# Optimization experiments

Hardware: AMD Instinct MI355X
Metric: run time of the kernel (lower is better)

## Reference

```python
import jax, jax.numpy as jnp
import numpy as np

B, T, C, H = 8, 2048, 256, 4
D = C // H  # head_dim = 64
SCALE = D ** -0.5


def setup_inputs() -> dict:
    key = jax.random.key(0)
    ks = jax.random.split(key, 5)
    return {
        "x": jax.random.normal(ks[0], (B, T, C), dtype=jnp.float32),
        "Wqkv": jax.random.normal(ks[1], (C, 3 * C), dtype=jnp.float32) * (C ** -0.5),
        "bqkv": jax.random.normal(ks[2], (3 * C,), dtype=jnp.float32) * 0.02,
        "Wproj": jax.random.normal(ks[3], (C, C), dtype=jnp.float32) * (C ** -0.5),
        "bproj": jax.random.normal(ks[4], (C,), dtype=jnp.float32) * 0.02,
    }


def reference(x, Wqkv, bqkv, Wproj, bproj):
    b, t, c = x.shape
    # QKV projection -> (3, B, H, T, D) matching torch permute(2,0,3,1,4)
    qkv = (x @ Wqkv + bqkv).reshape(b, t, 3, H, D)
    qkv = jnp.transpose(qkv, (2, 0, 3, 1, 4))
    q, k, v = qkv[0], qkv[1], qkv[2]  # each (B, H, T, D)
    # Full T x T scores (faithful to the original non-fused implementation)
    attn = jnp.einsum("bhqd,bhkd->bhqk", q, k) * SCALE
    causal = jnp.triu(jnp.ones((t, t), dtype=bool), k=1)  # True above diagonal
    attn = jnp.where(causal, -jnp.inf, attn)
    attn = jax.nn.softmax(attn, axis=-1)
    # dropout is identity in eval mode
    out = jnp.einsum("bhqk,bhkd->bhqd", attn, v)  # (B, H, T, D)
    out = jnp.transpose(out, (0, 2, 1, 3)).reshape(b, t, c)
    return out @ Wproj + bproj
```

## Files before the change

### kernel.cpp

```cpp
#include <hip/hip_runtime.h>
#include <hip/hip_bf16.h>
#include <math.h>

#define BATCH 8
#define SEQ   2048
#define CH    256
#define NH    4
#define HD    64
#define NQB   (SEQ / 64)
#define QSCALE 0.18033688011112042f

typedef short  bfrag  __attribute__((ext_vector_type(8)));
typedef float  ffrag  __attribute__((ext_vector_type(4)));
typedef float  facc16 __attribute__((ext_vector_type(16)));
typedef unsigned short ushort_t;
typedef unsigned int u32;

__device__ __forceinline__ unsigned short f2bf(float f) {
    union { float f; unsigned int u; } v; v.f = f;
    unsigned int r = v.u + 0x7FFF + ((v.u >> 16) & 1);
    return (unsigned short)(r >> 16);
}
__device__ __forceinline__ unsigned int pack2(float a, float b) {
    const __hip_bfloat162 p = __float22bfloat162_rn(make_float2(a, b));
    return *(const unsigned int*)&p;
}
__device__ __forceinline__ void gload16(const ushort_t* g, ushort_t* l) {
    __builtin_amdgcn_global_load_lds(
        (const __attribute__((address_space(1))) u32*)g,
        (__attribute__((address_space(3))) u32*)l, 16, 0, 0);
}
__device__ __forceinline__ void half_swap(u32& a, u32& b) {
#if __has_builtin(__builtin_amdgcn_permlane32_swap)
    auto r = __builtin_amdgcn_permlane32_swap(a, b, false, false);
    a = r[0]; b = r[1];
#else
    const u32 sa = (u32)__shfl_xor((int)a, 32);
    const u32 sb = (u32)__shfl_xor((int)b, 32);
    const bool hi = (threadIdx.x & 32) != 0;
    const u32 na = hi ? sb : a;
    const u32 nb = hi ? b : sa;
    a = na; b = nb;
#endif
}

#define WQN (CH * 3 * CH)
#define WPN (CH * CH)
#define XN  (BATCH * SEQ * CH)
#define XN8 (XN / 8)

__global__ __launch_bounds__(256) void prep_kernel(
    const float* __restrict__ x,
    const float* __restrict__ Wqkv, const float* __restrict__ Wproj,
    ushort_t* __restrict__ xb,
    ushort_t* __restrict__ WqkvT, ushort_t* __restrict__ WprojT) {
    const int fid = blockIdx.x * 256 + threadIdx.x;
    if (fid < XN8) {
        const float4 a = *(const float4*)&x[(size_t)fid * 8];
        const float4 c = *(const float4*)&x[(size_t)fid * 8 + 4];
        uint4 pk;
        pk.x = pack2(a.x, a.y); pk.y = pack2(a.z, a.w);
        pk.z = pack2(c.x, c.y); pk.w = pack2(c.z, c.w);
        *(uint4*)&xb[(size_t)fid * 8] = pk;
    } else {
        const int id = fid - XN8;
        if (id < WQN) {
            const int n = id >> 8, k = id & 255;
            WqkvT[n * CH + k] = f2bf(Wqkv[k * (3 * CH) + n]);
        } else if (id < WQN + WPN) {
            const int i = id - WQN;
            const int n = i >> 8, k = i & 255;
            WprojT[n * CH + k] = f2bf(Wproj[k * CH + n]);
        }
    }
}

#define GLS 72

__global__ __launch_bounds__(256) void qkv_mfma_kernel(
    const ushort_t* __restrict__ xb, const ushort_t* __restrict__ Wt,
    const float* __restrict__ bias,
    ushort_t* __restrict__ Qb, ushort_t* __restrict__ Kb,
    ushort_t* __restrict__ Vtb) {
    __shared__ ushort_t smem[128 * 136];
    ushort_t* As = smem;
    ushort_t* Bs = smem + 128 * 64;

    const int tid = threadIdx.x;
    const int wv  = tid >> 6;
    const int ln  = tid & 63;
    const int l15 = ln & 15;
    const int l4  = ln >> 4;
    const int e   = l15 & 7;
    const int wr  = wv >> 1;
    const int wc  = wv & 1;

    const int bid  = blockIdx.x;
    const int work = (bid & 7) * 96 + (bid >> 3);
    const int mt   = work / 6;
    const int nt   = work - mt * 6;
    const int n0   = nt * 128;
    const int m0   = mt * 128;

    const int grow = ln >> 3;
    const int swz  = ((ln & 7) ^ grow) * 8;

    ffrag acc[4][4];
    #pragma unroll
    for (int i = 0; i < 4; i++)
        #pragma unroll
        for (int j = 0; j < 4; j++) acc[i][j] = (ffrag){0.f, 0.f, 0.f, 0.f};

    for (int k0 = 0; k0 < CH; k0 += 64) {
        #pragma unroll
        for (int i = 0; i < 4; i++) {
            const int rowA = (i * 4 + wv) * 8 + grow;
            gload16(&xb[(size_t)(m0 + rowA) * CH + k0 + swz], &As[(i * 4 + wv) * 512]);
            gload16(&Wt[(size_t)(n0 + rowA) * CH + k0 + swz], &Bs[(i * 4 + wv) * 512]);
        }
        __syncthreads();
        #pragma unroll
        for (int kk = 0; kk < 64; kk += 32) {
            bfrag a[4], b[4];
            #pragma unroll
            for (int i = 0; i < 4; i++) {
                const int R = wr * 64 + i * 16 + l15;
                a[i] = *(const bfrag*)&As[R * 64 + ((((kk >> 3) + l4) ^ e) * 8)];
            }
            #pragma unroll
            for (int j = 0; j < 4; j++) {
                const int R = wc * 64 + j * 16 + l15;
                b[j] = *(const bfrag*)&Bs[R * 64 + ((((kk >> 3) + l4) ^ e) * 8)];
            }
            #pragma unroll
            for (int i = 0; i < 4; i++)
                #pragma unroll
                for (int j = 0; j < 4; j++)
                    acc[i][j] = __builtin_amdgcn_mfma_f32_16x16x32_bf16(a[i], b[j], acc[i][j], 0, 0, 0);
        }
        __syncthreads();
    }

    const int mat = n0 >> 8;
    const int b   = m0 >> 11;
    const int t0  = m0 & (SEQ - 1);
    ushort_t (*T)[136] = (ushort_t(*)[136])smem;

    if (mat < 2) {
        const float sc = (mat == 0) ? QSCALE : 1.0f;
        #pragma unroll
        for (int j = 0; j < 4; j++) {
            const int n_local = wc * 64 + j * 16 + l15;
            const float bj = bias[n0 + n_local];
            #pragma unroll
            for (int i = 0; i < 4; i++) {
                const int m_base = wr * 64 + i * 16 + l4 * 4;
                #pragma unroll
                for (int r = 0; r < 4; r++)
                    T[m_base + r][n_local] = f2bf((acc[i][j][r] + bj) * sc);
            }
        }
        __syncthreads();
        ushort_t* dst = (mat == 0) ? Qb : Kb;
        #pragma unroll
        for (int rr = 0; rr < 8; rr++) {
            const int fid = tid + rr * 256;
            const int row = fid >> 4;
            const int c8  = (fid & 15) * 8;
            const int n_glob = n0 + c8;
            const int h = (n_glob >> 6) & 3;
            const int d = n_glob & 63;
            *(uint4*)&dst[((size_t)((b * NH + h) * SEQ) + t0 + row) * HD + d] =
                *(const uint4*)&T[row][c8];
        }
    } else {
        #pragma unroll
        for (int j = 0; j < 4; j++) {
            const int n_local = wc * 64 + j * 16 + l15;
            const float bj = bias[n0 + n_local];
            #pragma unroll
            for (int i = 0; i < 4; i++) {
                const int m_base = wr * 64 + i * 16 + l4 * 4;
                ushort4 pk;
                pk.x = f2bf(acc[i][j][0] + bj);
                pk.y = f2bf(acc[i][j][1] + bj);
                pk.z = f2bf(acc[i][j][2] + bj);
                pk.w = f2bf(acc[i][j][3] + bj);
                *(ushort4*)&T[n_local][m_base] = pk;
            }
        }
        __syncthreads();
        #pragma unroll
        for (int rr = 0; rr < 8; rr++) {
            const int fid = tid + rr * 256;
            const int row = fid >> 4;
            const int c8  = (fid & 15) * 8;
            const int n_glob = n0 + row;
            const int h = (n_glob >> 6) & 3;
            const int d = n_glob & 63;
            *(uint4*)&Vtb[(size_t)((b * NH + h) * HD + d) * SEQ + t0 + c8] =
                *(const uint4*)&T[row][c8];
        }
    }
}

__global__ __launch_bounds__(256, 4) void attn_mfma_kernel(
    const ushort_t* __restrict__ Qb, const ushort_t* __restrict__ Kb,
    const ushort_t* __restrict__ Vtb, ushort_t* __restrict__ out) {
    __shared__ ushort_t KV[4 * 64 * 64];

    const int tid = threadIdx.x;
    const int wv  = tid >> 6;
    const int ln  = tid & 63;
    const int l31 = ln & 31;
    const int hi  = ln >> 5;
    const int qh  = wv >> 1;
    const int kh  = wv & 1;
    const int e8  = l31 & 7;

    const int L  = blockIdx.x;
    const int g  = L & 255;
    const int s4 = L >> 8;
    const int v  = g >> 5;
    const int qb = (s4 == 0) ? (31 - v) : (s4 == 1) ? (16 + v) : (s4 == 2) ? (15 - v) : v;
    const int bh = g & 31;
    const int b  = bh >> 2;
    const int h  = bh & 3;

    const ushort_t* Qp = Qb + ((size_t)(bh * SEQ + qb * 64 + qh * 32 + l31)) * HD + hi * 8;
    bfrag bq[4];
    #pragma unroll
    for (int s = 0; s < 4; s++) bq[s] = *(const bfrag*)(Qp + s * 16);

    const ushort_t* Kbase = Kb  + (size_t)bh * SEQ * HD;
    const ushort_t* Vbase = Vtb + (size_t)bh * HD * SEQ;
    const int srow  = tid >> 3;
    const int sc    = tid & 7;
    const int goffA = srow * 64 + sc * 8;
    const int voffA = srow * SEQ + sc * 8;
    const int soffA = srow * 64 + ((sc ^ (srow & 7)) * 8);

    const int krow = kh * 32 + l31;

    uint4 kK0, kK1, kV0, kV1;
    kK0 = *(const uint4*)&Kbase[goffA];
    kK1 = *(const uint4*)&Kbase[goffA + 32 * 64];
    kV0 = *(const uint4*)&Vbase[voffA];
    kV1 = *(const uint4*)&Vbase[voffA + 32 * SEQ];
    *(uint4*)&KV[soffA]          = kK0;
    *(uint4*)&KV[soffA + 2048]   = kK1;
    *(uint4*)&KV[8192 + soffA]        = kV0;
    *(uint4*)&KV[8192 + soffA + 2048] = kV1;
    if (qb >= 1) {
        kK0 = *(const uint4*)&Kbase[4096 + goffA];
        kK1 = *(const uint4*)&Kbase[4096 + goffA + 32 * 64];
        kV0 = *(const uint4*)&Vbase[64 + voffA];
        kV1 = *(const uint4*)&Vbase[64 + voffA + 32 * SEQ];
    }

    facc16 o0, o1;
    #pragma unroll
    for (int r = 0; r < 16; r++) { o0[r] = 0.f; o1[r] = 0.f; }
    float l_q = 0.f;
    const int qg_l = qb * 64 + qh * 32 + l31;

    for (int kt = 0; kt <= qb; kt++) {
        if (kt > 0) {
            const int kb = (kt & 1) * 4096;
            *(uint4*)&KV[kb + soffA]          = kK0;
            *(uint4*)&KV[kb + soffA + 2048]   = kK1;
            *(uint4*)&KV[8192 + kb + soffA]        = kV0;
            *(uint4*)&KV[8192 + kb + soffA + 2048] = kV1;
            if (kt < qb) {
                const ushort_t* Kp  = Kbase + (kt + 1) * 4096;
                const ushort_t* Vtp = Vbase + (kt + 1) * 64;
                kK0 = *(const uint4*)&Kp[goffA];
                kK1 = *(const uint4*)&Kp[goffA + 32 * 64];
                kV0 = *(const uint4*)&Vtp[voffA];
                kV1 = *(const uint4*)&Vtp[voffA + 32 * SEQ];
            }
        }
        __syncthreads();

        const ushort_t* Kbuf = KV + (kt & 1) * 4096;
        const ushort_t* Vbuf = KV + 8192 + (kt & 1) * 4096;

        facc16 s_;
        #pragma unroll
        for (int r = 0; r < 16; r++) s_[r] = 0.f;
        __builtin_amdgcn_s_setprio(1);
        #pragma unroll
        for (int s = 0; s < 4; s++) {
            const bfrag ak = *(const bfrag*)&Kbuf[krow * 64 + (((2 * s + hi) ^ e8) * 8)];
            s_ = __builtin_amdgcn_mfma_f32_32x32x16_bf16(ak, bq[s], s_, 0, 0, 0);
        }
        __builtin_amdgcn_s_setprio(0);

        if (kt == qb) {
            #pragma unroll
            for (int r = 0; r < 16; r++) {
                const int kabs = kt * 64 + kh * 32 + (r & 3) + 8 * (r >> 2) + 4 * hi;
                if (kabs > qg_l) s_[r] = -INFINITY;
            }
        }

        float p[16];
        #pragma unroll
        for (int r = 0; r < 16; r++) {
            p[r] = __builtin_amdgcn_exp2f(s_[r]);
            l_q += p[r];
        }

        __builtin_amdgcn_s_setprio(1);
        #pragma unroll
        for (int gstep = 0; gstep < 2; gstep++) {
            u32 A0 = pack2(p[8 * gstep + 0], p[8 * gstep + 1]);
            u32 A1 = pack2(p[8 * gstep + 2], p[8 * gstep + 3]);
            u32 B0 = pack2(p[8 * gstep + 4], p[8 * gstep + 5]);
            u32 B1 = pack2(p[8 * gstep + 6], p[8 * gstep + 7]);
            half_swap(A0, B0);
            half_swap(A1, B1);
            union { u32 w[4]; bfrag f; } pa;
            pa.w[0] = A0; pa.w[1] = A1; pa.w[2] = B0; pa.w[3] = B1;
            const int vc = ((kh * 4 + 2 * gstep + hi) ^ e8) * 8;
            const bfrag av0 = *(const bfrag*)&Vbuf[l31 * 64 + vc];
            const bfrag av1 = *(const bfrag*)&Vbuf[(32 + l31) * 64 + vc];
            o0 = __builtin_amdgcn_mfma_f32_32x32x16_bf16(av0, pa.f, o0, 0, 0, 0);
            o1 = __builtin_amdgcn_mfma_f32_32x32x16_bf16(av1, pa.f, o1, 0, 0, 0);
        }
        __builtin_amdgcn_s_setprio(0);
    }

    l_q += __shfl_xor(l_q, 32);

    __syncthreads();
    float* Xf = (float*)KV;
    const int xbase = qh * 2304 + ln * 36;
    if (kh) {
        #pragma unroll
        for (int gr = 0; gr < 4; gr++) {
            *(float4*)&Xf[xbase + gr * 4] =
                make_float4(o0[gr * 4], o0[gr * 4 + 1], o0[gr * 4 + 2], o0[gr * 4 + 3]);
            *(float4*)&Xf[xbase + 16 + gr * 4] =
                make_float4(o1[gr * 4], o1[gr * 4 + 1], o1[gr * 4 + 2], o1[gr * 4 + 3]);
        }
        Xf[4608 + qh * 64 + ln] = l_q;
    }
    __syncthreads();
    if (!kh) {
        #pragma unroll
        for (int gr = 0; gr < 4; gr++) {
            const float4 v0 = *(const float4*)&Xf[xbase + gr * 4];
            o0[gr * 4]     += v0.x; o0[gr * 4 + 1] += v0.y;
            o0[gr * 4 + 2] += v0.z; o0[gr * 4 + 3] += v0.w;
            const float4 v1 = *(const float4*)&Xf[xbase + 16 + gr * 4];
            o1[gr * 4]     += v1.x; o1[gr * 4 + 1] += v1.y;
            o1[gr * 4 + 2] += v1.z; o1[gr * 4 + 3] += v1.w;
        }
        l_q += Xf[4608 + qh * 64 + ln];

        const float li = 1.0f / l_q;
        const int tq = qb * 64 + qh * 32 + l31;
        ushort_t* op = out + (size_t)(b * SEQ + tq) * CH + h * HD;
        #pragma unroll
        for (int gr = 0; gr < 4; gr++) {
            const int d0a = gr * 8 + 4 * hi;
            ushort4 pk0;
            pk0.x = f2bf(o0[gr * 4]     * li);
            pk0.y = f2bf(o0[gr * 4 + 1] * li);
            pk0.z = f2bf(o0[gr * 4 + 2] * li);
            pk0.w = f2bf(o0[gr * 4 + 3] * li);
            *(ushort4*)&op[d0a] = pk0;
            ushort4 pk1;
            pk1.x = f2bf(o1[gr * 4]     * li);
            pk1.y = f2bf(o1[gr * 4 + 1] * li);
            pk1.z = f2bf(o1[gr * 4 + 2] * li);
            pk1.w = f2bf(o1[gr * 4 + 3] * li);
            *(ushort4*)&op[32 + d0a] = pk1;
        }
    }
}

__global__ __launch_bounds__(256) void proj_mfma_kernel(
    const ushort_t* __restrict__ Ab, const ushort_t* __restrict__ Wt,
    const float* __restrict__ bias, float* __restrict__ O) {
    __shared__ __align__(16) char smem_raw[128 * 68 * 4];
    ushort_t* As = (ushort_t*)smem_raw;
    ushort_t* Bs = As + 128 * GLS;

    const int tid = threadIdx.x;
    const int wv  = tid >> 6;
    const int ln  = tid & 63;
    const int l15 = ln & 15;
    const int l4  = ln >> 4;
    const int wr  = wv >> 1;
    const int wc  = wv & 1;

    const int bid  = blockIdx.x;
    const int work = (bid & 7) * 64 + (bid >> 3);
    const int mt   = work >> 2;
    const int nt   = work & 3;
    const int n0   = nt * 64;
    const int m0   = mt * 128;

    ffrag acc[4][2];
    #pragma unroll
    for (int i = 0; i < 4; i++)
        #pragma unroll
        for (int j = 0; j < 2; j++) acc[i][j] = (ffrag){0.f, 0.f, 0.f, 0.f};

    for (int k0 = 0; k0 < CH; k0 += 64) {
        #pragma unroll
        for (int r = 0; r < 4; r++) {
            const int fid = tid + r * 256;
            const int row = fid >> 3, c8 = (fid & 7) * 8;
            *(uint4*)&As[row * GLS + c8] = *(const uint4*)&Ab[(size_t)(m0 + row) * CH + k0 + c8];
        }
        #pragma unroll
        for (int r = 0; r < 2; r++) {
            const int fid = tid + r * 256;
            const int row = fid >> 3, c8 = (fid & 7) * 8;
            *(uint4*)&Bs[row * GLS + c8] = *(const uint4*)&Wt[(n0 + row) * CH + k0 + c8];
        }
        __syncthreads();
        #pragma unroll
        for (int kk = 0; kk < 64; kk += 32) {
            bfrag a[4], b[2];
            #pragma unroll
            for (int i = 0; i < 4; i++)
                a[i] = *(const bfrag*)&As[(wr * 64 + i * 16 + l15) * GLS + kk + l4 * 8];
            #pragma unroll
            for (int j = 0; j < 2; j++)
                b[j] = *(const bfrag*)&Bs[(wc * 32 + j * 16 + l15) * GLS + kk + l4 * 8];
            #pragma unroll
            for (int i = 0; i < 4; i++)
                #pragma unroll
                for (int j = 0; j < 2; j++)
                    acc[i][j] = __builtin_amdgcn_mfma_f32_16x16x32_bf16(a[i], b[j], acc[i][j], 0, 0, 0);
        }
        __syncthreads();
    }

    float (*Tf)[68] = (float(*)[68])smem_raw;
    #pragma unroll
    for (int j = 0; j < 2; j++) {
        const int n_local = wc * 32 + j * 16 + l15;
        const float bj = bias[n0 + n_local];
        #pragma unroll
        for (int i = 0; i < 4; i++) {
            const int m_base = wr * 64 + i * 16 + l4 * 4;
            #pragma unroll
            for (int r = 0; r < 4; r++)
                Tf[m_base + r][n_local] = acc[i][j][r] + bj;
        }
    }
    __syncthreads();
    #pragma unroll
    for (int rr = 0; rr < 8; rr++) {
        const int fid = tid + rr * 256;
        const int row = fid >> 4;
        const int c4  = (fid & 15) * 4;
        *(float4*)&O[(size_t)(m0 + row) * CH + n0 + c4] =
            *(const float4*)&Tf[row][c4];
    }
}

extern "C" void kernel_launch(void* const* d_in, const int* in_sizes, int n_in,
                              void* d_out, int out_size, void* d_ws, size_t ws_size,
                              hipStream_t stream) {
    const float* x     = (const float*)d_in[0];
    const float* Wqkv  = (const float*)d_in[1];
    const float* bqkv  = (const float*)d_in[2];
    const float* Wproj = (const float*)d_in[3];
    const float* bproj = (const float*)d_in[4];
    float* out = (float*)d_out;

    const size_t BHTD = (size_t)BATCH * NH * SEQ * HD;
    ushort_t* WqkvT  = (ushort_t*)d_ws;
    ushort_t* WprojT = WqkvT + (size_t)3 * CH * CH;
    ushort_t* Qb     = WprojT + (size_t)CH * CH;
    ushort_t* Kb     = Qb + BHTD;
    ushort_t* Vtb    = Kb + BHTD;
    ushort_t* attn_b = Vtb + BHTD;
    ushort_t* xb     = attn_b;

    {
        const int total = XN8 + WQN + WPN;
        prep_kernel<<<(total + 255) / 256, 256, 0, stream>>>(x, Wqkv, Wproj, xb, WqkvT, WprojT);
    }
    {
        qkv_mfma_kernel<<<dim3(768), 256, 0, stream>>>(xb, WqkvT, bqkv, Qb, Kb, Vtb);
    }
    {
        attn_mfma_kernel<<<dim3(NQB * BATCH * NH), 256, 0, stream>>>(Qb, Kb, Vtb, attn_b);
    }
    {
        proj_mfma_kernel<<<dim3(512), 256, 0, stream>>>(attn_b, WprojT, bproj, out);
    }
}
```

Baseline: 126.3 us.

## Register-prefetch next K-tile in QKV and output projection GEMMs

Both projection GEMMs now load the next 64-wide K slice from global memory into registers while the current slice is computed from LDS. The QKV kernel drops direct global-to-LDS loads (global_load_lds) in favour of register staging with explicit ds_write, and gains a launch-bounds occupancy hint of 3 blocks per CU. This aims to hide global load latency behind MFMA work, at the cost of extra registers and an extra LDS write pass.

New measurement: 153.9 us. +21.9%, slower.

```diff
diff --git a/kernel.cpp b/kernel.cpp
--- a/kernel.cpp
+++ b/kernel.cpp
@@ -24,11 +24,6 @@
 __device__ __forceinline__ unsigned int pack2(float a, float b) {
     const __hip_bfloat162 p = __float22bfloat162_rn(make_float2(a, b));
     return *(const unsigned int*)&p;
-}
-__device__ __forceinline__ void gload16(const ushort_t* g, ushort_t* l) {
-    __builtin_amdgcn_global_load_lds(
-        (const __attribute__((address_space(1))) u32*)g,
-        (__attribute__((address_space(3))) u32*)l, 16, 0, 0);
 }
 __device__ __forceinline__ void half_swap(u32& a, u32& b) {
 #if __has_builtin(__builtin_amdgcn_permlane32_swap)
@@ -77,7 +72,7 @@
 
 #define GLS 72
 
-__global__ __launch_bounds__(256) void qkv_mfma_kernel(
+__global__ __launch_bounds__(256, 3) void qkv_mfma_kernel(
     const ushort_t* __restrict__ xb, const ushort_t* __restrict__ Wt,
     const float* __restrict__ bias,
     ushort_t* __restrict__ Qb, ushort_t* __restrict__ Kb,
@@ -104,6 +99,7 @@
 
     const int grow = ln >> 3;
     const int swz  = ((ln & 7) ^ grow) * 8;
+    const int cch  = (ln & 7) * 8;
 
     ffrag acc[4][4];
     #pragma unroll
@@ -111,12 +107,29 @@
         #pragma unroll
         for (int j = 0; j < 4; j++) acc[i][j] = (ffrag){0.f, 0.f, 0.f, 0.f};
 
-    for (int k0 = 0; k0 < CH; k0 += 64) {
+    uint4 rA[4], rB[4];
+    #pragma unroll
+    for (int i = 0; i < 4; i++) {
+        const int rowA = (i * 4 + wv) * 8 + grow;
+        rA[i] = *(const uint4*)&xb[(size_t)(m0 + rowA) * CH + swz];
+        rB[i] = *(const uint4*)&Wt[(size_t)(n0 + rowA) * CH + swz];
+    }
+
+    for (int s = 0; s < 4; s++) {
         #pragma unroll
         for (int i = 0; i < 4; i++) {
-            const int rowA = (i * 4 + wv) * 8 + grow;
-            gload16(&xb[(size_t)(m0 + rowA) * CH + k0 + swz], &As[(i * 4 + wv) * 512]);
-            gload16(&Wt[(size_t)(n0 + rowA) * CH + k0 + swz], &Bs[(i * 4 + wv) * 512]);
+            const int rbase = (i * 4 + wv) * 512 + grow * 64 + cch;
+            *(uint4*)&As[rbase] = rA[i];
+            *(uint4*)&Bs[rbase] = rB[i];
+        }
+        if (s < 3) {
+            const int k0n = (s + 1) * 64;
+            #pragma unroll
+            for (int i = 0; i < 4; i++) {
+                const int rowA = (i * 4 + wv) * 8 + grow;
+                rA[i] = *(const uint4*)&xb[(size_t)(m0 + rowA) * CH + k0n + swz];
+                rB[i] = *(const uint4*)&Wt[(size_t)(n0 + rowA) * CH + k0n + swz];
+            }
         }
         __syncthreads();
         #pragma unroll
@@ -409,18 +422,47 @@
         #pragma unroll
         for (int j = 0; j < 2; j++) acc[i][j] = (ffrag){0.f, 0.f, 0.f, 0.f};
 
-    for (int k0 = 0; k0 < CH; k0 += 64) {
+    uint4 rA[4], rB[2];
+    #pragma unroll
+    for (int r = 0; r < 4; r++) {
+        const int fid = tid + r * 256;
+        const int row = fid >> 3, c8 = (fid & 7) * 8;
+        rA[r] = *(const uint4*)&Ab[(size_t)(m0 + row) * CH + c8];
+    }
+    #pragma unroll
+    for (int r = 0; r < 2; r++) {
+        const int fid = tid + r * 256;
+        const int row = fid >> 3, c8 = (fid & 7) * 8;
+        rB[r] = *(const uint4*)&Wt[(size_t)(n0 + row) * CH + c8];
+    }
+
+    for (int s = 0; s < 4; s++) {
         #pragma unroll
         for (int r = 0; r < 4; r++) {
             const int fid = tid + r * 256;
             const int row = fid >> 3, c8 = (fid & 7) * 8;
-            *(uint4*)&As[row * GLS + c8] = *(const uint4*)&Ab[(size_t)(m0 + row) * CH + k0 + c8];
+            *(uint4*)&As[row * GLS + c8] = rA[r];
         }
         #pragma unroll
         for (int r = 0; r < 2; r++) {
             const int fid = tid + r * 256;
             const int row = fid >> 3, c8 = (fid & 7) * 8;
-            *(uint4*)&Bs[row * GLS + c8] = *(const uint4*)&Wt[(n0 + row) * CH + k0 + c8];
+            *(uint4*)&Bs[row * GLS + c8] = rB[r];
+        }
+        if (s < 3) {
+            const int k0n = (s + 1) * 64;
+            #pragma unroll
+            for (int r = 0; r < 4; r++) {
+                const int fid = tid + r * 256;
+                const int row = fid >> 3, c8 = (fid & 7) * 8;
+                rA[r] = *(const uint4*)&Ab[(size_t)(m0 + row) * CH + k0n + c8];
+            }
+            #pragma unroll
+            for (int r = 0; r < 2; r++) {
+                const int fid = tid + r * 256;
+                const int row = fid >> 3, c8 = (fid & 7) * 8;
+                rB[r] = *(const uint4*)&Wt[(size_t)(n0 + row) * CH + k0n + c8];
+            }
         }
         __syncthreads();
         #pragma unroll
```
